# Kernel tuning notes

Hardware: AMD Instinct MI355X
Metric: run time of the kernel (lower is better)

Reference implementation:

```python
import jax, jax.numpy as jnp
import numpy as np

N = 20000      # nodes
E = 320000     # edges (avg degree 16)
D = 256        # embedding_dim
H = 8          # num_heads
DH = D // H    # head_dim = 32
ED = 64        # edge_dim
FF = 4 * D     # feed-forward hidden
EPS = 1e-5


def setup_inputs() -> dict:
    key = jax.random.key(0)
    ks = jax.random.split(key, 32)

    def lin_w(k, i, o):
        return (jax.random.normal(k, (i, o), jnp.float32) / np.sqrt(i)).astype(jnp.float32)

    return {
        "x": jax.random.normal(ks[0], (N, D), jnp.float32),
        "edge_features": jax.random.normal(ks[1], (E, ED), jnp.float32),
        "edge_weights": jax.random.uniform(ks[2], (E,), jnp.float32),
        "edge_index": jax.random.randint(ks[3], (2, E), 0, N, dtype=jnp.int32),
        "Wq": lin_w(ks[4], D, D), "bq": jnp.zeros((D,), jnp.float32),
        "Wk": lin_w(ks[5], D, D), "bk": jnp.zeros((D,), jnp.float32),
        "Wv": lin_w(ks[6], D, D), "bv": jnp.zeros((D,), jnp.float32),
        "We": lin_w(ks[7], ED, DH), "be": jnp.zeros((DH,), jnp.float32),
        "Wo": lin_w(ks[8], D, D), "bo": jnp.zeros((D,), jnp.float32),
        "ln1_g": jnp.ones((D,), jnp.float32), "ln1_b": jnp.zeros((D,), jnp.float32),
        "ln2_g": jnp.ones((D,), jnp.float32), "ln2_b": jnp.zeros((D,), jnp.float32),
        "W1": lin_w(ks[9], D, FF), "b1": jnp.zeros((FF,), jnp.float32),
        "W2": lin_w(ks[10], FF, D), "b2": jnp.zeros((D,), jnp.float32),
        "alpha": jnp.ones((1,), jnp.float32),
        "beta": jnp.ones((1,), jnp.float32),
    }


def _layernorm(x, g, b):
    m = jnp.mean(x, axis=-1, keepdims=True)
    v = jnp.var(x, axis=-1, keepdims=True)
    return (x - m) * jax.lax.rsqrt(v + EPS) * g + b


def _edge_attention(xn, edge_index, ef, ew, Wq, bq, Wk, bk, Wv, bv, We, be, Wo, bo):
    n = xn.shape[0]
    scale = DH ** -0.5
    q = (xn @ Wq + bq).reshape(n, H, DH)
    k = (xn @ Wk + bk).reshape(n, H, DH)
    v = (xn @ Wv + bv).reshape(n, H, DH)
    src, dst = edge_index[0], edge_index[1]
    ep = ef @ We + be                               # [E, DH], shared across heads
    # per-edge, per-head scores: q[dst] . (k[src] + edge_proj)
    scores = jnp.einsum('ehd,ehd->eh', q[dst], k[src] + ep[:, None, :]) * scale
    scores = scores * ew[:, None]
    # segment softmax over incoming edges of each dst node
    m = jax.ops.segment_max(scores, dst, num_segments=n)
    m = jnp.where(jnp.isfinite(m), m, 0.0)          # nodes with no incoming edges
    ex = jnp.exp(scores - m[dst])
    s = jax.ops.segment_sum(ex, dst, num_segments=n)
    attn = ex / s[dst]                              # [E, H]
    # scatter-weighted V aggregation; nodes with no edges stay zero (matches torch)
    out = jax.ops.segment_sum(attn[:, :, None] * v[src], dst, num_segments=n)
    out = out.reshape(n, D) @ Wo + bo
    return out


def reference(x, edge_features, edge_weights, edge_index,
              Wq, bq, Wk, bk, Wv, bv, We, be, Wo, bo,
              ln1_g, ln1_b, ln2_g, ln2_b, W1, b1, W2, b2, alpha, beta):
    xn = _layernorm(x, ln1_g, ln1_b)
    attn_out = _edge_attention(xn, edge_index, edge_features, edge_weights,
                               Wq, bq, Wk, bk, Wv, bv, We, be, Wo, bo)
    x = x + alpha * attn_out
    xn = _layernorm(x, ln2_g, ln2_b)
    ff = jax.nn.gelu(xn @ W1 + b1, approximate=False) @ W2 + b2
    x = x + beta * ff
    return x
```

## Files before the change

### kernel.cpp

```cpp
#include <hip/hip_runtime.h>
#include <math.h>

#define NN 20000
#define EE 320000
#define DD 256
#define HH 8
#define DHD 32
#define EDF 64
#define FFD 1024

typedef unsigned short u16;
typedef __attribute__((ext_vector_type(8))) __bf16 bf16x8;
typedef __attribute__((ext_vector_type(4))) float f32x4;

#define XN_OFF   (0)
#define AGGB_OFF (2560000)
#define X1_OFF   (5120000)
#define QKV_OFF  (10240000)
#define EP_OFF   (25600000)
#define WT_OFF   (35840000)
#define BQKV_OFF (36240000)
#define CSR_OFF  (36250000)

__device__ __forceinline__ u16 f2bf(float f) {
    unsigned u = __float_as_uint(f);
    return (u16)((u + 0x7FFFu + ((u >> 16) & 1u)) >> 16);
}
__device__ __forceinline__ float bf2f(u16 h) {
    return __uint_as_float(((unsigned)h) << 16);
}
__device__ __forceinline__ float gelu_exact(float v) {
    return 0.5f * v * (1.0f + erff(v * 0.70710678118654752f));
}

#define GLDS16(g, l) __builtin_amdgcn_global_load_lds(             \
    (__attribute__((address_space(1))) void*)(g),                  \
    (__attribute__((address_space(3))) void*)(l), 16, 0, 0)

__global__ __launch_bounds__(256) void ln_kernel(const float* __restrict__ x,
                                                 const float* __restrict__ g,
                                                 const float* __restrict__ b,
                                                 u16* __restrict__ out) {
    int row = blockIdx.x * 4 + (threadIdx.x >> 6);
    if (row >= NN) return;
    int lane = threadIdx.x & 63;
    float4 v = *(const float4*)&x[(size_t)row * DD + lane * 4];
    float s  = v.x + v.y + v.z + v.w;
    float ss = v.x * v.x + v.y * v.y + v.z * v.z + v.w * v.w;
    #pragma unroll
    for (int o = 32; o >= 1; o >>= 1) {
        s  += __shfl_xor(s, o);
        ss += __shfl_xor(ss, o);
    }
    float mean = s * (1.0f / DD);
    float var  = ss * (1.0f / DD) - mean * mean;
    float inv  = rsqrtf(var + 1e-5f);
    float4 gg = *(const float4*)&g[lane * 4];
    float4 bb = *(const float4*)&b[lane * 4];
    ushort4 o4;
    o4.x = f2bf((v.x - mean) * inv * gg.x + bb.x);
    o4.y = f2bf((v.y - mean) * inv * gg.y + bb.y);
    o4.z = f2bf((v.z - mean) * inv * gg.z + bb.z);
    o4.w = f2bf((v.w - mean) * inv * gg.w + bb.w);
    *(ushort4*)&out[(size_t)row * DD + lane * 4] = o4;
}

__device__ __forceinline__ void convw_body(const float* __restrict__ src,
                                           u16* __restrict__ dst, int K, int N,
                                           int vb) {
    int n = vb * 4 + (threadIdx.x >> 6);
    int lane = threadIdx.x & 63;
    if (n >= N) return;
    for (int k = lane * 4; k < K; k += 256) {
        ushort4 o;
        o.x = f2bf(src[(size_t)(k + 0) * N + n]);
        o.y = f2bf(src[(size_t)(k + 1) * N + n]);
        o.z = f2bf(src[(size_t)(k + 2) * N + n]);
        o.w = f2bf(src[(size_t)(k + 3) * N + n]);
        *(ushort4*)&dst[(size_t)n * K + k] = o;
    }
}

__global__ __launch_bounds__(256) void prep_kernel(
    const float* __restrict__ Wq, const float* __restrict__ Wk,
    const float* __restrict__ Wv, const float* __restrict__ Wo,
    const float* __restrict__ W1, const float* __restrict__ W2,
    const float* __restrict__ We,
    const float* __restrict__ bq, const float* __restrict__ bk,
    const float* __restrict__ bv,
    u16* __restrict__ WqkvT, u16* __restrict__ WoT, u16* __restrict__ W1T,
    u16* __restrict__ W2T, u16* __restrict__ WeT, float* __restrict__ bqkv) {
    int b = blockIdx.x;
    if      (b < 64)  convw_body(Wq, WqkvT,            256, 256,  b);
    else if (b < 128) convw_body(Wk, WqkvT + 65536,    256, 256,  b - 64);
    else if (b < 192) convw_body(Wv, WqkvT + 131072,   256, 256,  b - 128);
    else if (b < 256) convw_body(Wo, WoT,              256, 256,  b - 192);
    else if (b < 512) convw_body(W1, W1T,              256, 1024, b - 256);
    else if (b < 576) convw_body(W2, W2T,              1024, 256, b - 512);
    else if (b < 584) convw_body(We, WeT,              64,  32,   b - 576);
    else {
        int t = threadIdx.x;
        bqkv[t] = bq[t];
        bqkv[256 + t] = bk[t];
        bqkv[512 + t] = bv[t];
    }
}

template <int BM, int BN, int EPI>
__global__ __launch_bounds__(256) void gemm_bf16(
    const u16* __restrict__ A, const u16* __restrict__ BT,
    const float* __restrict__ bias,
    float* __restrict__ Cf, u16* __restrict__ Cb,
    const float* __restrict__ res, const float* __restrict__ scale,
    int M, int K, int N)
{
    constexpr int FM = BM / 32, FN = BN / 32;
    constexpr int nA = BM / 32, nB = BN / 32;
    constexpr int NST = (nA > nB) ? nA : nB;
    __shared__ u16 Asm[BM * 64];
    __shared__ u16 Bsm[BN * 64];
    const int tid  = threadIdx.x;
    const int lane = tid & 63;
    const int w    = tid >> 6;
    const int wr   = w >> 1, wc = w & 1;
    const int bm   = blockIdx.x * BM;
    const int bn   = blockIdx.y * BN;

    f32x4 acc[FM][FN] = {};

    int st_row[NST], st_src[NST], st_dst[NST];
    #pragma unroll
    for (int i = 0; i < NST; i++) {
        int base  = i * 4096 + w * 1024;
        int off   = base + lane * 16;
        int row   = off >> 7;
        int inner = off & 127;
        st_row[i] = row;
        st_src[i] = (inner ^ ((row & 7) << 4)) >> 1;
        st_dst[i] = base;
    }
    const int arow0 = wr * (BM / 2) + (lane & 15);
    const int brow0 = wc * (BN / 2) + (lane & 15);
    const int kb0   = (lane >> 4) * 16;

    for (int k0 = 0; k0 < K; k0 += 64) {
        #pragma unroll
        for (int i = 0; i < nA; i++) {
            int r = bm + st_row[i]; if (r > M - 1) r = M - 1;
            GLDS16(A + (size_t)r * K + k0 + st_src[i], (char*)Asm + st_dst[i]);
        }
        #pragma unroll
        for (int i = 0; i < nB; i++) {
            int r = bn + st_row[i];
            GLDS16(BT + (size_t)r * K + k0 + st_src[i], (char*)Bsm + st_dst[i]);
        }
        asm volatile("s_waitcnt vmcnt(0)" ::: "memory");
        __syncthreads();
        #pragma unroll
        for (int s = 0; s < 2; s++) {
            bf16x8 af[FM], bfv[FN];
            #pragma unroll
            for (int i = 0; i < FM; i++) {
                int row  = arow0 + i * 16;
                int byte = (row << 7) + ((kb0 + s * 64) ^ ((row & 7) << 4));
                af[i] = *(const bf16x8*)((const char*)Asm + byte);
            }
            #pragma unroll
            for (int j = 0; j < FN; j++) {
                int row  = brow0 + j * 16;
                int byte = (row << 7) + ((kb0 + s * 64) ^ ((row & 7) << 4));
                bfv[j] = *(const bf16x8*)((const char*)Bsm + byte);
            }
            #pragma unroll
            for (int i = 0; i < FM; i++)
                #pragma unroll
                for (int j = 0; j < FN; j++)
                    acc[i][j] = __builtin_amdgcn_mfma_f32_16x16x32_bf16(
                        af[i], bfv[j], acc[i][j], 0, 0, 0);
        }
        __syncthreads();
    }

    float sc = 0.f;
    if constexpr (EPI == 2) sc = scale[0];
    const int col0 = bn + wc * (BN / 2) + (lane & 15);
    const int row0 = bm + wr * (BM / 2) + ((lane >> 4) << 2);
    #pragma unroll
    for (int i = 0; i < FM; i++) {
        #pragma unroll
        for (int j = 0; j < FN; j++) {
            int col = col0 + j * 16;
            float bb = bias[col];
            #pragma unroll
            for (int r = 0; r < 4; r++) {
                int row = row0 + i * 16 + r;
                if (row < M) {
                    float o = acc[i][j][r] + bb;
                    if constexpr (EPI == 1) {
                        Cb[(size_t)row * N + col] = f2bf(gelu_exact(o));
                    } else if constexpr (EPI == 2) {
                        Cf[(size_t)row * N + col] = res[(size_t)row * N + col] + sc * o;
                    } else if constexpr (EPI == 3) {
                        if (col < 256) {
                            Cb[(size_t)row * 256 + col] = f2bf(o * 0.17677669529663689f);
                        } else if (col < 512) {
                            Cb[(size_t)NN * 256 + (size_t)row * 512 + (col - 256) * 2] = f2bf(o);
                        } else {
                            Cb[(size_t)NN * 256 + (size_t)row * 512 + (col - 512) * 2 + 1] = f2bf(o);
                        }
                    } else {
                        Cf[(size_t)row * N + col] = o;
                    }
                }
            }
        }
    }
}

__global__ __launch_bounds__(256) void ep_mfma(const float* __restrict__ ef,
                                               const u16* __restrict__ WeT,
                                               const float* __restrict__ be,
                                               const int* __restrict__ epos,
                                               u16* __restrict__ epc) {
    const int lane = threadIdx.x & 63;
    const int wv   = threadIdx.x >> 6;
    const int e0   = blockIdx.x * 64 + wv * 16;
    const int ar   = lane & 15;
    const int k8   = (lane >> 4) * 8;

    f32x4 acc[2] = {};
    #pragma unroll
    for (int s = 0; s < 2; s++) {
        const float* ap = ef + (size_t)(e0 + ar) * EDF + s * 32 + k8;
        float4 a0 = *(const float4*)ap;
        float4 a1 = *(const float4*)(ap + 4);
        bf16x8 af;
        af[0] = (__bf16)a0.x; af[1] = (__bf16)a0.y; af[2] = (__bf16)a0.z; af[3] = (__bf16)a0.w;
        af[4] = (__bf16)a1.x; af[5] = (__bf16)a1.y; af[6] = (__bf16)a1.z; af[7] = (__bf16)a1.w;
        #pragma unroll
        for (int j = 0; j < 2; j++) {
            bf16x8 bf = *(const bf16x8*)&WeT[(size_t)(j * 16 + ar) * EDF + s * 32 + k8];
            acc[j] = __builtin_amdgcn_mfma_f32_16x16x32_bf16(af, bf, acc[j], 0, 0, 0);
        }
    }
    const int row0 = (lane >> 4) << 2;
    #pragma unroll
    for (int r = 0; r < 4; r++) {
        int pos = epos[e0 + row0 + r];
        #pragma unroll
        for (int j = 0; j < 2; j++) {
            int col = j * 16 + ar;
            epc[(size_t)pos * DHD + col] = f2bf(acc[j][r] + be[col]);
        }
    }
}

__global__ __launch_bounds__(256) void count_kernel(const int* __restrict__ ei,
                                                    int* __restrict__ counts) {
    int e = blockIdx.x * 256 + threadIdx.x;
    if (e >= EE) return;
    atomicAdd(&counts[ei[EE + e]], 1);
}

__global__ __launch_bounds__(1024) void scan_kernel(const int* __restrict__ counts,
                                                    int* __restrict__ row_start,
                                                    int* __restrict__ cursor) {
    __shared__ int part[1024];
    const int CH = 20;
    int t = threadIdx.x;
    int base = t * CH;
    int loc[CH];
    int s = 0;
    #pragma unroll
    for (int i = 0; i < CH; i++) {
        int idx = base + i;
        int c = (idx < NN) ? counts[idx] : 0;
        loc[i] = s;
        s += c;
    }
    part[t] = s;
    __syncthreads();
    for (int o = 1; o < 1024; o <<= 1) {
        int vv = (t >= o) ? part[t - o] : 0;
        __syncthreads();
        part[t] += vv;
        __syncthreads();
    }
    int off = (t > 0) ? part[t - 1] : 0;
    #pragma unroll
    for (int i = 0; i < CH; i++) {
        int idx = base + i;
        if (idx < NN) {
            int rs = off + loc[i];
            row_start[idx] = rs;
            cursor[idx] = rs;
        }
    }
    if (t == 1023) row_start[NN] = part[1023];
}

__global__ __launch_bounds__(256) void fill_kernel(const int* __restrict__ ei,
                                                   const float* __restrict__ ew,
                                                   int* __restrict__ cursor,
                                                   int2* __restrict__ csr,
                                                   int* __restrict__ epos) {
    int e = blockIdx.x * 256 + threadIdx.x;
    if (e >= EE) return;
    int src = ei[e];
    int dst = ei[EE + e];
    int pos = atomicAdd(&cursor[dst], 1);
    csr[pos] = make_int2(src, __float_as_int(ew[e] * 1.44269504088896f));
    epos[e] = pos;
}

__global__ __launch_bounds__(256) void attn_kernel(const u16* __restrict__ qb,
                                                   const u16* __restrict__ kv,
                                                   const u16* __restrict__ epc,
                                                   const int2* __restrict__ csr,
                                                   const int* __restrict__ row_start,
                                                   u16* __restrict__ aggb) {
    const int dst  = blockIdx.x * 4 + (threadIdx.x >> 6);
    const int lane = threadIdx.x & 63;
    const int g    = lane & 7;
    const int d0   = (lane >> 3) * 32 + g * 4;
    const int beg = row_start[dst];
    const int end = row_start[dst + 1];
    ushort4 q4 = *(const ushort4*)&qb[(size_t)dst * DD + d0];
    float4 qv = make_float4(bf2f(q4.x), bf2f(q4.y), bf2f(q4.z), bf2f(q4.w));
    float ss = 0.f;
    float4 acc = make_float4(0.f, 0.f, 0.f, 0.f);

    if (end > beg) {
        int2 pc[4];
        #pragma unroll
        for (int u = 0; u < 4; u++) pc[u] = csr[min(beg + u, end - 1)];
        for (int i = beg; i < end; i += 4) {
            int2 cur[4];
            #pragma unroll
            for (int u = 0; u < 4; u++) cur[u] = pc[u];
            ushort4 a[4], b[4], e4[4];
            #pragma unroll
            for (int u = 0; u < 4; u++) {
                const u16* kvr = &kv[(size_t)cur[u].x * 512 + d0 * 2];
                a[u]  = *(const ushort4*)kvr;
                b[u]  = *(const ushort4*)(kvr + 4);
                e4[u] = *(const ushort4*)&epc[(size_t)min(i + u, end - 1) * DHD + g * 4];
            }
            #pragma unroll
            for (int u = 0; u < 4; u++) pc[u] = csr[min(i + 4 + u, end - 1)];
            float pp[4];
            #pragma unroll
            for (int u = 0; u < 4; u++) {
                float k0 = bf2f(a[u].x) + bf2f(e4[u].x);
                float k1 = bf2f(a[u].z) + bf2f(e4[u].y);
                float k2 = bf2f(b[u].x) + bf2f(e4[u].z);
                float k3 = bf2f(b[u].z) + bf2f(e4[u].w);
                pp[u] = fmaf(qv.x, k0, fmaf(qv.y, k1, fmaf(qv.z, k2, qv.w * k3)));
            }
            #pragma unroll
            for (int o = 4; o >= 1; o >>= 1) {
                #pragma unroll
                for (int u = 0; u < 4; u++) pp[u] += __shfl_xor(pp[u], o);
            }
            #pragma unroll
            for (int u = 0; u < 4; u++) {
                float wq = (i + u < end)
                         ? exp2f(pp[u] * __int_as_float(cur[u].y)) : 0.f;
                ss += wq;
                acc.x = fmaf(wq, bf2f(a[u].y), acc.x);
                acc.y = fmaf(wq, bf2f(a[u].w), acc.y);
                acc.z = fmaf(wq, bf2f(b[u].y), acc.z);
                acc.w = fmaf(wq, bf2f(b[u].w), acc.w);
            }
        }
    }
    float inv = (end > beg) ? 1.f / ss : 0.f;
    ushort4 o4;
    o4.x = f2bf(acc.x * inv);
    o4.y = f2bf(acc.y * inv);
    o4.z = f2bf(acc.z * inv);
    o4.w = f2bf(acc.w * inv);
    *(ushort4*)&aggb[(size_t)dst * DD + d0] = o4;
}

extern "C" void kernel_launch(void* const* d_in, const int* in_sizes, int n_in,
                              void* d_out, int out_size, void* d_ws, size_t ws_size,
                              hipStream_t stream) {
    const float* x    = (const float*)d_in[0];
    const float* ef   = (const float*)d_in[1];
    const float* ew   = (const float*)d_in[2];
    const int*   ei   = (const int*)d_in[3];
    const float* Wq   = (const float*)d_in[4];
    const float* bq   = (const float*)d_in[5];
    const float* Wk   = (const float*)d_in[6];
    const float* bk   = (const float*)d_in[7];
    const float* Wv   = (const float*)d_in[8];
    const float* bv   = (const float*)d_in[9];
    const float* We   = (const float*)d_in[10];
    const float* be   = (const float*)d_in[11];
    const float* Wo   = (const float*)d_in[12];
    const float* bo   = (const float*)d_in[13];
    const float* ln1g = (const float*)d_in[14];
    const float* ln1b = (const float*)d_in[15];
    const float* ln2g = (const float*)d_in[16];
    const float* ln2b = (const float*)d_in[17];
    const float* W1   = (const float*)d_in[18];
    const float* b1   = (const float*)d_in[19];
    const float* W2   = (const float*)d_in[20];
    const float* b2   = (const float*)d_in[21];
    const float* alpha = (const float*)d_in[22];
    const float* beta  = (const float*)d_in[23];

    float* ws    = (float*)d_ws;
    u16*   xn    = (u16*)(ws + XN_OFF);
    u16*   aggb  = (u16*)(ws + AGGB_OFF);
    float* x1    = ws + X1_OFF;
    u16*   qb    = (u16*)(ws + QKV_OFF);
    u16*   kv    = qb + (size_t)NN * 256;
    u16*   ff1   = (u16*)(ws + QKV_OFF);
    u16*   epc   = (u16*)(ws + EP_OFF);
    u16*   wt    = (u16*)(ws + WT_OFF);
    u16*   WqkvT = wt;
    u16*   WoT   = wt + 768 * 256;
    u16*   W1T   = WoT + 256 * 256;
    u16*   W2T   = W1T + 1024 * 256;
    u16*   WeT   = W2T + 256 * 1024;
    float* bqkv  = ws + BQKV_OFF;
    float* out   = (float*)d_out;

    int*  counts    = (int*)(ws + CSR_OFF);
    int*  row_start = counts + NN;
    int*  cursor    = row_start + NN + 1;
    int2* csr       = (int2*)(counts + 60002);
    int*  epos      = counts + 60002 + 2 * EE;

    hipMemsetAsync(counts, 0, (size_t)NN * sizeof(int), stream);

    prep_kernel<<<585, 256, 0, stream>>>(Wq, Wk, Wv, Wo, W1, W2, We, bq, bk, bv,
                                         WqkvT, WoT, W1T, W2T, WeT, bqkv);

    count_kernel<<<EE / 256, 256, 0, stream>>>(ei, counts);
    scan_kernel<<<1, 1024, 0, stream>>>(counts, row_start, cursor);
    fill_kernel<<<EE / 256, 256, 0, stream>>>(ei, ew, cursor, csr, epos);

    ln_kernel<<<NN / 4, 256, 0, stream>>>(x, ln1g, ln1b, xn);

    gemm_bf16<128, 128, 3><<<dim3(157, 6), 256, 0, stream>>>(
        xn, WqkvT, bqkv, nullptr, qb, nullptr, nullptr, NN, DD, 768);

    ep_mfma<<<EE / 64, 256, 0, stream>>>(ef, WeT, be, epos, epc);

    attn_kernel<<<NN / 4, 256, 0, stream>>>(qb, kv, epc, csr, row_start, aggb);

    gemm_bf16<64, 128, 2><<<dim3(313, 2), 256, 0, stream>>>(
        aggb, WoT, bo, x1, nullptr, x, alpha, NN, DD, DD);

    ln_kernel<<<NN / 4, 256, 0, stream>>>(x1, ln2g, ln2b, xn);

    gemm_bf16<128, 128, 1><<<dim3(157, 8), 256, 0, stream>>>(
        xn, W1T, b1, nullptr, ff1, nullptr, nullptr, NN, DD, FFD);
    gemm_bf16<64, 128, 2><<<dim3(313, 2), 256, 0, stream>>>(
        ff1, W2T, b2, out, nullptr, x1, beta, NN, FFD, DD);
}
```

Measured before the change: 301.7 us.

## Merge independent launches and restructure attention loop with aligned vector CSR loads

Combines weight prep, edge counting and the first layernorm into one launch, and the QKV GEMM plus edge-projection MFMA into another. This removes kernel launch gaps and lets independent work overlap. The attention inner loop now peels an unaligned first edge so CSR entries can be read as int4 pairs, loads K/V as 16-byte vectors, and drops the clamped prefetch and masking in favour of a scalar tail loop. The CSR offset is shifted for 16-byte alignment. The cost is that branchy merged kernels may lose occupancy because of the GEMM's shared memory and registers.

```diff
diff --git a/kernel.cpp b/kernel.cpp
--- a/kernel.cpp
+++ b/kernel.cpp
@@ -11,6 +11,7 @@
 
 typedef unsigned short u16;
 typedef __attribute__((ext_vector_type(8))) __bf16 bf16x8;
+typedef __attribute__((ext_vector_type(8))) unsigned short u16x8;
 typedef __attribute__((ext_vector_type(4))) float f32x4;
 
 #define XN_OFF   (0)
@@ -37,11 +38,11 @@
     (__attribute__((address_space(1))) void*)(g),                  \
     (__attribute__((address_space(3))) void*)(l), 16, 0, 0)
 
-__global__ __launch_bounds__(256) void ln_kernel(const float* __restrict__ x,
-                                                 const float* __restrict__ g,
-                                                 const float* __restrict__ b,
-                                                 u16* __restrict__ out) {
-    int row = blockIdx.x * 4 + (threadIdx.x >> 6);
+__device__ __forceinline__ void ln_body(const float* __restrict__ x,
+                                        const float* __restrict__ g,
+                                        const float* __restrict__ b,
+                                        u16* __restrict__ out, int vb) {
+    int row = vb * 4 + (threadIdx.x >> 6);
     if (row >= NN) return;
     int lane = threadIdx.x & 63;
     float4 v = *(const float4*)&x[(size_t)row * DD + lane * 4];
@@ -63,6 +64,13 @@
     o4.z = f2bf((v.z - mean) * inv * gg.z + bb.z);
     o4.w = f2bf((v.w - mean) * inv * gg.w + bb.w);
     *(ushort4*)&out[(size_t)row * DD + lane * 4] = o4;
+}
+
+__global__ __launch_bounds__(256) void ln_kernel(const float* __restrict__ x,
+                                                 const float* __restrict__ g,
+                                                 const float* __restrict__ b,
+                                                 u16* __restrict__ out) {
+    ln_body(x, g, b, out, blockIdx.x);
 }
 
 __device__ __forceinline__ void convw_body(const float* __restrict__ src,
@@ -81,7 +89,7 @@
     }
 }
 
-__global__ __launch_bounds__(256) void prep_kernel(
+__global__ __launch_bounds__(256) void prep_count_ln_kernel(
     const float* __restrict__ Wq, const float* __restrict__ Wk,
     const float* __restrict__ Wv, const float* __restrict__ Wo,
     const float* __restrict__ W1, const float* __restrict__ W2,
@@ -89,7 +97,10 @@
     const float* __restrict__ bq, const float* __restrict__ bk,
     const float* __restrict__ bv,
     u16* __restrict__ WqkvT, u16* __restrict__ WoT, u16* __restrict__ W1T,
-    u16* __restrict__ W2T, u16* __restrict__ WeT, float* __restrict__ bqkv) {
+    u16* __restrict__ W2T, u16* __restrict__ WeT, float* __restrict__ bqkv,
+    const int* __restrict__ ei, int* __restrict__ counts,
+    const float* __restrict__ x, const float* __restrict__ ln1g,
+    const float* __restrict__ ln1b, u16* __restrict__ xn) {
     int b = blockIdx.x;
     if      (b < 64)  convw_body(Wq, WqkvT,            256, 256,  b);
     else if (b < 128) convw_body(Wk, WqkvT + 65536,    256, 256,  b - 64);
@@ -98,21 +109,26 @@
     else if (b < 512) convw_body(W1, W1T,              256, 1024, b - 256);
     else if (b < 576) convw_body(W2, W2T,              1024, 256, b - 512);
     else if (b < 584) convw_body(We, WeT,              64,  32,   b - 576);
-    else {
+    else if (b < 585) {
         int t = threadIdx.x;
         bqkv[t] = bq[t];
         bqkv[256 + t] = bk[t];
         bqkv[512 + t] = bv[t];
+    } else if (b < 1835) {
+        int e = (b - 585) * 256 + threadIdx.x;
+        if (e < EE) atomicAdd(&counts[ei[EE + e]], 1);
+    } else {
+        ln_body(x, ln1g, ln1b, xn, b - 1835);
     }
 }
 
 template <int BM, int BN, int EPI>
-__global__ __launch_bounds__(256) void gemm_bf16(
+__device__ __forceinline__ void gemm_body(
     const u16* __restrict__ A, const u16* __restrict__ BT,
     const float* __restrict__ bias,
     float* __restrict__ Cf, u16* __restrict__ Cb,
     const float* __restrict__ res, const float* __restrict__ scale,
-    int M, int K, int N)
+    int M, int K, int N, int bxx, int byy)
 {
     constexpr int FM = BM / 32, FN = BN / 32;
     constexpr int nA = BM / 32, nB = BN / 32;
@@ -123,8 +139,8 @@
     const int lane = tid & 63;
     const int w    = tid >> 6;
     const int wr   = w >> 1, wc = w & 1;
-    const int bm   = blockIdx.x * BM;
-    const int bn   = blockIdx.y * BN;
+    const int bm   = bxx * BM;
+    const int bn   = byy * BN;
 
     f32x4 acc[FM][FN] = {};
 
@@ -217,14 +233,25 @@
     }
 }
 
-__global__ __launch_bounds__(256) void ep_mfma(const float* __restrict__ ef,
-                                               const u16* __restrict__ WeT,
-                                               const float* __restrict__ be,
-                                               const int* __restrict__ epos,
-                                               u16* __restrict__ epc) {
+template <int BM, int BN, int EPI>
+__global__ __launch_bounds__(256) void gemm_bf16(
+    const u16* __restrict__ A, const u16* __restrict__ BT,
+    const float* __restrict__ bias,
+    float* __restrict__ Cf, u16* __restrict__ Cb,
+    const float* __restrict__ res, const float* __restrict__ scale,
+    int M, int K, int N) {
+    gemm_body<BM, BN, EPI>(A, BT, bias, Cf, Cb, res, scale, M, K, N,
+                           blockIdx.x, blockIdx.y);
+}
+
+__device__ __forceinline__ void ep_body(const float* __restrict__ ef,
+                                        const u16* __restrict__ WeT,
+                                        const float* __restrict__ be,
+                                        const int* __restrict__ epos,
+                                        u16* __restrict__ epc, int blk) {
     const int lane = threadIdx.x & 63;
     const int wv   = threadIdx.x >> 6;
-    const int e0   = blockIdx.x * 64 + wv * 16;
+    const int e0   = blk * 64 + wv * 16;
     const int ar   = lane & 15;
     const int k8   = (lane >> 4) * 8;
 
@@ -255,11 +282,19 @@
     }
 }
 
-__global__ __launch_bounds__(256) void count_kernel(const int* __restrict__ ei,
-                                                    int* __restrict__ counts) {
-    int e = blockIdx.x * 256 + threadIdx.x;
-    if (e >= EE) return;
-    atomicAdd(&counts[ei[EE + e]], 1);
+__global__ __launch_bounds__(256) void qkv_ep_kernel(
+    const u16* __restrict__ xn, const u16* __restrict__ WqkvT,
+    const float* __restrict__ bqkv, u16* __restrict__ qb,
+    const float* __restrict__ ef, const u16* __restrict__ WeT,
+    const float* __restrict__ be, const int* __restrict__ epos,
+    u16* __restrict__ epc) {
+    int b = blockIdx.x;
+    if (b < 942) {
+        gemm_body<128, 128, 3>(xn, WqkvT, bqkv, nullptr, qb, nullptr, nullptr,
+                               NN, DD, 768, b % 157, b / 157);
+    } else {
+        ep_body(ef, WeT, be, epos, epc, b - 942);
+    }
 }
 
 __global__ __launch_bounds__(1024) void scan_kernel(const int* __restrict__ counts,
@@ -330,49 +365,80 @@
     float ss = 0.f;
     float4 acc = make_float4(0.f, 0.f, 0.f, 0.f);
 
-    if (end > beg) {
-        int2 pc[4];
-        #pragma unroll
-        for (int u = 0; u < 4; u++) pc[u] = csr[min(beg + u, end - 1)];
-        for (int i = beg; i < end; i += 4) {
-            int2 cur[4];
+    int i = beg;
+    if ((i & 1) && i < end) {
+        int2 p = csr[i];
+        u16x8 kk = *(const u16x8*)&kv[(size_t)p.x * 512 + d0 * 2];
+        ushort4 e4 = *(const ushort4*)&epc[(size_t)i * DHD + g * 4];
+        float k0 = bf2f(kk[0]) + bf2f(e4.x);
+        float k1 = bf2f(kk[2]) + bf2f(e4.y);
+        float k2 = bf2f(kk[4]) + bf2f(e4.z);
+        float k3 = bf2f(kk[6]) + bf2f(e4.w);
+        float pv = fmaf(qv.x, k0, fmaf(qv.y, k1, fmaf(qv.z, k2, qv.w * k3)));
+        #pragma unroll
+        for (int o = 4; o >= 1; o >>= 1) pv += __shfl_xor(pv, o);
+        float wq = exp2f(pv * __int_as_float(p.y));
+        ss += wq;
+        acc.x = fmaf(wq, bf2f(kk[1]), acc.x);
+        acc.y = fmaf(wq, bf2f(kk[3]), acc.y);
+        acc.z = fmaf(wq, bf2f(kk[5]), acc.z);
+        acc.w = fmaf(wq, bf2f(kk[7]), acc.w);
+        ++i;
+    }
+    for (; i + 4 <= end; i += 4) {
+        int4 c01 = *(const int4*)&csr[i];
+        int4 c23 = *(const int4*)&csr[i + 2];
+        int   sr[4] = {c01.x, c01.z, c23.x, c23.z};
+        float wt[4] = {__int_as_float(c01.y), __int_as_float(c01.w),
+                       __int_as_float(c23.y), __int_as_float(c23.w)};
+        u16x8 kk[4];
+        ushort4 e4[4];
+        #pragma unroll
+        for (int u = 0; u < 4; u++) {
+            kk[u] = *(const u16x8*)&kv[(size_t)sr[u] * 512 + d0 * 2];
+            e4[u] = *(const ushort4*)&epc[(size_t)(i + u) * DHD + g * 4];
+        }
+        float pp[4];
+        #pragma unroll
+        for (int u = 0; u < 4; u++) {
+            float k0 = bf2f(kk[u][0]) + bf2f(e4[u].x);
+            float k1 = bf2f(kk[u][2]) + bf2f(e4[u].y);
+            float k2 = bf2f(kk[u][4]) + bf2f(e4[u].z);
+            float k3 = bf2f(kk[u][6]) + bf2f(e4[u].w);
+            pp[u] = fmaf(qv.x, k0, fmaf(qv.y, k1, fmaf(qv.z, k2, qv.w * k3)));
+        }
+        #pragma unroll
+        for (int o = 4; o >= 1; o >>= 1) {
             #pragma unroll
-            for (int u = 0; u < 4; u++) cur[u] = pc[u];
-            ushort4 a[4], b[4], e4[4];
-            #pragma unroll
-            for (int u = 0; u < 4; u++) {
-                const u16* kvr = &kv[(size_t)cur[u].x * 512 + d0 * 2];
-                a[u]  = *(const ushort4*)kvr;
-                b[u]  = *(const ushort4*)(kvr + 4);
-                e4[u] = *(const ushort4*)&epc[(size_t)min(i + u, end - 1) * DHD + g * 4];
-            }
-            #pragma unroll
-            for (int u = 0; u < 4; u++) pc[u] = csr[min(i + 4 + u, end - 1)];
-            float pp[4];
-            #pragma unroll
-            for (int u = 0; u < 4; u++) {
-                float k0 = bf2f(a[u].x) + bf2f(e4[u].x);
-                float k1 = bf2f(a[u].z) + bf2f(e4[u].y);
-                float k2 = bf2f(b[u].x) + bf2f(e4[u].z);
-                float k3 = bf2f(b[u].z) + bf2f(e4[u].w);
-                pp[u] = fmaf(qv.x, k0, fmaf(qv.y, k1, fmaf(qv.z, k2, qv.w * k3)));
-            }
-            #pragma unroll
-            for (int o = 4; o >= 1; o >>= 1) {
-                #pragma unroll
-                for (int u = 0; u < 4; u++) pp[u] += __shfl_xor(pp[u], o);
-            }
-            #pragma unroll
-            for (int u = 0; u < 4; u++) {
-                float wq = (i + u < end)
-                         ? exp2f(pp[u] * __int_as_float(cur[u].y)) : 0.f;
-                ss += wq;
-                acc.x = fmaf(wq, bf2f(a[u].y), acc.x);
-                acc.y = fmaf(wq, bf2f(a[u].w), acc.y);
-                acc.z = fmaf(wq, bf2f(b[u].y), acc.z);
-                acc.w = fmaf(wq, bf2f(b[u].w), acc.w);
-            }
-        }
+            for (int u = 0; u < 4; u++) pp[u] += __shfl_xor(pp[u], o);
+        }
+        #pragma unroll
+        for (int u = 0; u < 4; u++) {
+            float wq = exp2f(pp[u] * wt[u]);
+            ss += wq;
+            acc.x = fmaf(wq, bf2f(kk[u][1]), acc.x);
+            acc.y = fmaf(wq, bf2f(kk[u][3]), acc.y);
+            acc.z = fmaf(wq, bf2f(kk[u][5]), acc.z);
+            acc.w = fmaf(wq, bf2f(kk[u][7]), acc.w);
+        }
+    }
+    for (; i < end; ++i) {
+        int2 p = csr[i];
+        u16x8 kk = *(const u16x8*)&kv[(size_t)p.x * 512 + d0 * 2];
+        ushort4 e4 = *(const ushort4*)&epc[(size_t)i * DHD + g * 4];
+        float k0 = bf2f(kk[0]) + bf2f(e4.x);
+        float k1 = bf2f(kk[2]) + bf2f(e4.y);
+        float k2 = bf2f(kk[4]) + bf2f(e4.z);
+        float k3 = bf2f(kk[6]) + bf2f(e4.w);
+        float pv = fmaf(qv.x, k0, fmaf(qv.y, k1, fmaf(qv.z, k2, qv.w * k3)));
+        #pragma unroll
+        for (int o = 4; o >= 1; o >>= 1) pv += __shfl_xor(pv, o);
+        float wq = exp2f(pv * __int_as_float(p.y));
+        ss += wq;
+        acc.x = fmaf(wq, bf2f(kk[1]), acc.x);
+        acc.y = fmaf(wq, bf2f(kk[3]), acc.y);
+        acc.z = fmaf(wq, bf2f(kk[5]), acc.z);
+        acc.w = fmaf(wq, bf2f(kk[7]), acc.w);
     }
     float inv = (end > beg) ? 1.f / ss : 0.f;
     ushort4 o4;
@@ -431,24 +497,20 @@
     int*  counts    = (int*)(ws + CSR_OFF);
     int*  row_start = counts + NN;
     int*  cursor    = row_start + NN + 1;
-    int2* csr       = (int2*)(counts + 60002);
-    int*  epos      = counts + 60002 + 2 * EE;
+    int2* csr       = (int2*)(counts + 60004);
+    int*  epos      = counts + 60004 + 2 * EE;
 
     hipMemsetAsync(counts, 0, (size_t)NN * sizeof(int), stream);
 
-    prep_kernel<<<585, 256, 0, stream>>>(Wq, Wk, Wv, Wo, W1, W2, We, bq, bk, bv,
-                                         WqkvT, WoT, W1T, W2T, WeT, bqkv);
-
-    count_kernel<<<EE / 256, 256, 0, stream>>>(ei, counts);
+    prep_count_ln_kernel<<<6835, 256, 0, stream>>>(
+        Wq, Wk, Wv, Wo, W1, W2, We, bq, bk, bv,
+        WqkvT, WoT, W1T, W2T, WeT, bqkv, ei, counts, x, ln1g, ln1b, xn);
+
     scan_kernel<<<1, 1024, 0, stream>>>(counts, row_start, cursor);
     fill_kernel<<<EE / 256, 256, 0, stream>>>(ei, ew, cursor, csr, epos);
 
-    ln_kernel<<<NN / 4, 256, 0, stream>>>(x, ln1g, ln1b, xn);
-
-    gemm_bf16<128, 128, 3><<<dim3(157, 6), 256, 0, stream>>>(
-        xn, WqkvT, bqkv, nullptr, qb, nullptr, nullptr, NN, DD, 768);
-
-    ep_mfma<<<EE / 64, 256, 0, stream>>>(ef, WeT, be, epos, epc);
+    qkv_ep_kernel<<<5942, 256, 0, stream>>>(xn, WqkvT, bqkv, qb,
+                                            ef, WeT, be, epos, epc);
 
     attn_kernel<<<NN / 4, 256, 0, stream>>>(qb, kv, epc, csr, row_start, aggb);
 
```

Result: faster. 269.9 us (-10.6%).
